# Performance work log

Measured on AMD Instinct MI355X. Metric: run time of the kernel, lower is better.

The kernel has to match this reference:

```python
import jax, jax.numpy as jnp
import numpy as np

N, S, E, D = 20000, 4096, 640000, 256
SPARSITY = 0.02  # fraction of nonzero entries in the normalized matrix


def setup_inputs() -> dict:
    key = jax.random.key(0)
    ks = jax.random.split(key, 6)
    u = jax.random.uniform(ks[0], (N, S), dtype=jnp.float32)
    init = jnp.where(u < SPARSITY, u, 0.0)
    edge_index = jax.random.randint(ks[1], (2, E), 0, N, dtype=jnp.int32)
    edge_attr = jax.random.uniform(ks[2], (E,), dtype=jnp.float32)
    # Projection MLP params (Linear(1,16) -> ReLU -> Linear(16,D))
    w1 = jax.random.normal(ks[3], (1, 16), dtype=jnp.float32)
    b1 = jnp.zeros((16,), dtype=jnp.float32)
    w2 = jax.random.normal(ks[4], (16, D), dtype=jnp.float32) / np.float32(np.sqrt(16))
    b2 = jnp.zeros((D,), dtype=jnp.float32)
    # GCN weight (xavier-ish)
    W = jax.random.normal(ks[5], (D, D), dtype=jnp.float32) / np.float32(np.sqrt(D))
    return {"init": init, "edge_index": edge_index, "edge_attr": edge_attr,
            "w1": w1, "b1": b1, "w2": w2, "b2": b2, "W": W}


def reference(init, edge_index, edge_attr, w1, b1, w2, b2, W):
    n, s = init.shape
    # Projection: torch code feeds the nonzero COLUMN INDICES (as floats) of each
    # row through the MLP and means them. Vectorized: precompute MLP(j) for all
    # column indices j, then do a masked mean via a single matmul.
    idx = jnp.arange(s, dtype=init.dtype)[:, None]          # [S,1]
    phi = jax.nn.relu(idx @ w1 + b1) @ w2 + b2              # [S,D]
    mask = (init != 0).astype(init.dtype)                   # [N,S]
    cnt = mask.sum(axis=1)                                  # [N]
    # rows with zero nonzeros yield zero embedding (matches torch branch)
    h = (mask @ phi) / jnp.maximum(cnt, 1.0)[:, None]       # [N,D]

    # 3-layer GCN: scatter_add of h[row]*attr into col, then mm + relu
    row, col = edge_index[0], edge_index[1]
    for _ in range(3):
        h_agg = jax.ops.segment_sum(h[row] * edge_attr[:, None], col,
                                    num_segments=n)          # [N,D]
        h = jax.nn.relu(h_agg @ W)
    return h
```

## Files before the change

### kernel.cpp

```cpp
#include <hip/hip_runtime.h>


#define N_NODES 20000
#define S_COLS  4096
#define E_EDGES 640000
#define D_DIM   256

typedef unsigned short bf16_t;
typedef __attribute__((ext_vector_type(8))) short short8;
typedef __attribute__((ext_vector_type(4))) float f32x4;

__device__ __forceinline__ float bf2f(bf16_t u) {
    union { unsigned int i; float f; } v; v.i = ((unsigned int)u) << 16; return v.f;
}
__device__ __forceinline__ bf16_t f2bf(float x) {
    union { float f; unsigned int i; } v; v.f = x;
    unsigned int r = v.i + 0x7FFF + ((v.i >> 16) & 1);
    return (bf16_t)(r >> 16);
}
__device__ __forceinline__ float lo_bf(unsigned int u) {
    union { unsigned int i; float f; } v; v.i = u << 16; return v.f;
}
__device__ __forceinline__ float hi_bf(unsigned int u) {
    union { unsigned int i; float f; } v; v.i = u & 0xFFFF0000u; return v.f;
}
__device__ __forceinline__ unsigned int pack_bf(float a, float b) {
    return (unsigned int)f2bf(a) | ((unsigned int)f2bf(b) << 16);
}

__global__ void __launch_bounds__(256, 4)
mega_kernel(const float* __restrict__ init_m,
            const float* __restrict__ w1, const float* __restrict__ b1,
            const float* __restrict__ w2, const float* __restrict__ b2,
            bf16_t* __restrict__ h,
            const int* __restrict__ eidx, int* __restrict__ cnt,
            const float* __restrict__ W,
            bf16_t* __restrict__ Wt_hi, bf16_t* __restrict__ Wt_lo) {
    int b = blockIdx.x;
    int t = threadIdx.x;

    if (b >= 5000) {
        int bb = b - 5000;
        if (bb < 2500) {
            int e = bb * 256 + t;
            atomicAdd(&cnt[eidx[E_EDGES + e]], 1);
        } else {
            int k = bb - 2500;
            float w = W[k * D_DIM + t];
            bf16_t hi = f2bf(w);
            bf16_t lo = f2bf(w - bf2f(hi));
            Wt_hi[t * D_DIM + k] = hi;
            Wt_lo[t * D_DIM + k] = lo;
        }
        return;
    }

    __shared__ float w2s[16][256];
#pragma unroll
    for (int k = 0; k < 16; ++k) w2s[k][t] = w2[k * D_DIM + t];
    __syncthreads();

    int wave = t >> 6, lane = t & 63;
    int row  = b * 4 + wave;

    float lw1[16], lb1[16];
#pragma unroll
    for (int k = 0; k < 16; ++k) { lw1[k] = w1[k]; lb1[k] = b1[k]; }

    const float4* rowp = (const float4*)(init_m + (size_t)row * S_COLS);
    float f[16] = {};
    float cn = 0.f;

#define PROC_COMP(val, jb)                                            \
    if ((val) != 0.f) {                                               \
        float jf = (float)(jb);                                       \
        _Pragma("unroll")                                             \
        for (int k = 0; k < 16; ++k)                                  \
            f[k] += fmaxf(jf * lw1[k] + lb1[k], 0.f);                 \
        cn += 1.f;                                                    \
    }

#pragma unroll 4
    for (int v = 0; v < 16; ++v) {
        float4 x = rowp[v * 64 + lane];
        int jb = (v * 64 + lane) * 4;
        PROC_COMP(x.x, jb)
        PROC_COMP(x.y, jb + 1)
        PROC_COMP(x.z, jb + 2)
        PROC_COMP(x.w, jb + 3)
    }
#undef PROC_COMP

#pragma unroll
    for (int off = 32; off > 0; off >>= 1) {
#pragma unroll
        for (int k = 0; k < 16; ++k) f[k] += __shfl_xor(f[k], off, 64);
        cn += __shfl_xor(cn, off, 64);
    }

    float4 b2v = *(const float4*)(b2 + 4 * lane);
    float o0 = cn * b2v.x, o1 = cn * b2v.y, o2 = cn * b2v.z, o3 = cn * b2v.w;
#pragma unroll
    for (int k = 0; k < 16; ++k) {
        float4 wv = *(const float4*)(&w2s[k][4 * lane]);
        o0 += f[k] * wv.x;  o1 += f[k] * wv.y;
        o2 += f[k] * wv.z;  o3 += f[k] * wv.w;
    }
    float inv = 1.f / fmaxf(cn, 1.f);
    uint2 o;
    o.x = pack_bf(o0 * inv, o1 * inv);
    o.y = pack_bf(o2 * inv, o3 * inv);
    *(uint2*)(h + (size_t)row * D_DIM + 4 * lane) = o;
}

__global__ void scan_kernel(const int* __restrict__ cnt, int* __restrict__ offs,
                            int* __restrict__ cur) {
    __shared__ int sdata[1024];
    int t = threadIdx.x;
    int base = t * 20;
    int vals[20];
    int local = 0;
#pragma unroll
    for (int k = 0; k < 20; ++k) {
        int idx = base + k;
        int v = (idx < N_NODES) ? cnt[idx] : 0;
        vals[k] = local;
        local += v;
    }
    sdata[t] = local;
    __syncthreads();
    for (int off = 1; off < 1024; off <<= 1) {
        int v = (t >= off) ? sdata[t - off] : 0;
        __syncthreads();
        sdata[t] += v;
        __syncthreads();
    }
    int prefix = (t == 0) ? 0 : sdata[t - 1];
#pragma unroll
    for (int k = 0; k < 20; ++k) {
        int idx = base + k;
        if (idx < N_NODES) {
            int o = prefix + vals[k];
            offs[idx] = o;
            cur[idx]  = o;
        }
    }
    if (t == 1023) offs[N_NODES] = sdata[1023];
}

__global__ void fill_kernel(const int* __restrict__ eidx, const float* __restrict__ attr,
                            int* __restrict__ cur, int* __restrict__ src_s,
                            float* __restrict__ attr_s) {
    int e = blockIdx.x * 256 + threadIdx.x;
    if (e < E_EDGES) {
        int r = eidx[e];
        int c = eidx[E_EDGES + e];
        int pos = atomicAdd(&cur[c], 1);
        src_s[pos]  = r;
        attr_s[pos] = attr[e];
    }
}

__global__ void gather_kernel(const bf16_t* __restrict__ h,
                              const int* __restrict__ offs,
                              const int* __restrict__ src_s,
                              const float* __restrict__ attr_s,
                              bf16_t* __restrict__ g) {
    int wid  = (blockIdx.x * blockDim.x + threadIdx.x) >> 6;
    int lane = threadIdx.x & 63;
    if (wid >= N_NODES) return;
    int half = lane >> 5;
    int l32  = lane & 31;
    int e0 = offs[wid], e1 = offs[wid + 1];

    float acc[8] = {};
    for (int base = e0; base < e1; base += 64) {
        int n = e1 - base; if (n > 64) n = 64;
        int   r_l = 0; float a_l = 0.f;
        if (lane < n) { r_l = src_s[base + lane]; a_l = attr_s[base + lane]; }
        int nn = (n + 15) & ~15;
        for (int q = 0; q < nn; q += 16) {
#pragma unroll
            for (int u = 0; u < 8; ++u) {
                int   sl = q + 2 * u + half;
                int   r  = __shfl(r_l, sl, 64);
                float a  = __shfl(a_l, sl, 64);
                uint4 v  = ((const uint4*)(h + (size_t)r * D_DIM))[l32];
                acc[0] += lo_bf(v.x) * a;  acc[1] += hi_bf(v.x) * a;
                acc[2] += lo_bf(v.y) * a;  acc[3] += hi_bf(v.y) * a;
                acc[4] += lo_bf(v.z) * a;  acc[5] += hi_bf(v.z) * a;
                acc[6] += lo_bf(v.w) * a;  acc[7] += hi_bf(v.w) * a;
            }
        }
    }
#pragma unroll
    for (int i = 0; i < 8; ++i) acc[i] += __shfl_xor(acc[i], 32, 64);

    if (half == 0) {
        uint4 o;
        o.x = pack_bf(acc[0], acc[1]);
        o.y = pack_bf(acc[2], acc[3]);
        o.z = pack_bf(acc[4], acc[5]);
        o.w = pack_bf(acc[6], acc[7]);
        ((uint4*)(g + (size_t)wid * D_DIM))[l32] = o;
    }
}

__global__ void __launch_bounds__(256, 2)
gemm_relu_kernel(const bf16_t* __restrict__ g,
                 const bf16_t* __restrict__ Wt_hi,
                 const bf16_t* __restrict__ Wt_lo,
                 bf16_t* __restrict__ hdst, float* __restrict__ fdst) {
    __shared__ bf16_t Bs[64][512];
    int tid  = threadIdx.x;
    int w    = tid >> 6;
    int lane = tid & 63;
    int quad = lane >> 4;
    int id16 = lane & 15;

    int d    = blockIdx.x;
    int xcd  = d & 7;
    int base = (xcd < 4) ? xcd * 79 : 316 + (xcd - 4) * 78;
    int wg   = base + (d >> 3);
    int bx   = wg >> 2;
    int by   = wg & 3;
    int bn   = by * 64;
    int bm0  = bx * 128;

    char* bs = (char*)Bs;

    {
        int tn0 = tid >> 4;
        int ts0 = tid & 15;
#pragma unroll
        for (int it = 0; it < 16; ++it) {
            int n   = tn0 + (it & 3) * 16;
            int seg = ts0 + (it >> 2) * 16;
            const bf16_t* src = (seg < 32 ? Wt_hi : Wt_lo)
                              + (size_t)(bn + n) * D_DIM + (seg & 31) * 8;
            unsigned off = (unsigned)(n * 1024 + seg * 16) ^ (unsigned)((n & 7) << 4);
            *(uint4*)(bs + off) = *(const uint4*)src;
        }
    }

    int r0 = bm0 + w * 32;
    short8 areg[2][8];
#pragma unroll
    for (int j = 0; j < 2; ++j) {
        const bf16_t* arow = g + (size_t)(r0 + j * 16 + id16) * D_DIM;
#pragma unroll
        for (int i = 0; i < 8; ++i)
            areg[j][i] = *(const short8*)(arow + i * 32 + quad * 8);
    }

    __syncthreads();

    unsigned swz   = (unsigned)((id16 & 7) << 4);
    unsigned nbase = (unsigned)(id16 * 1024);

    f32x4 acc[2][4];
#pragma unroll
    for (int j = 0; j < 2; ++j)
#pragma unroll
        for (int nt = 0; nt < 4; ++nt) acc[j][nt] = (f32x4){0.f, 0.f, 0.f, 0.f};

#pragma unroll
    for (int ks = 0; ks < 8; ++ks) {
        unsigned kb = ((unsigned)(ks * 64 + quad * 16)) ^ swz;
#pragma unroll
        for (int nt = 0; nt < 4; ++nt) {
            unsigned off = (unsigned)(nt * 16384) + nbase + kb;
            short8 bh = *(const short8*)(bs + off);
            short8 bl = *(const short8*)(bs + off + 512);
            acc[0][nt] = __builtin_amdgcn_mfma_f32_16x16x32_bf16(areg[0][ks], bh, acc[0][nt], 0, 0, 0);
            acc[0][nt] = __builtin_amdgcn_mfma_f32_16x16x32_bf16(areg[0][ks], bl, acc[0][nt], 0, 0, 0);
            acc[1][nt] = __builtin_amdgcn_mfma_f32_16x16x32_bf16(areg[1][ks], bh, acc[1][nt], 0, 0, 0);
            acc[1][nt] = __builtin_amdgcn_mfma_f32_16x16x32_bf16(areg[1][ks], bl, acc[1][nt], 0, 0, 0);
        }
    }

#pragma unroll
    for (int j = 0; j < 2; ++j) {
#pragma unroll
        for (int nt = 0; nt < 4; ++nt) {
#pragma unroll
            for (int r = 0; r < 4; ++r) {
                int m = r0 + j * 16 + quad * 4 + r;
                if (m < N_NODES) {
                    int n = bn + nt * 16 + id16;
                    float v = fmaxf(acc[j][nt][r], 0.f);
                    if (hdst) hdst[(size_t)m * D_DIM + n] = f2bf(v);
                    else      fdst[(size_t)m * D_DIM + n] = v;
                }
            }
        }
    }
}

extern "C" void kernel_launch(void* const* d_in, const int* in_sizes, int n_in,
                              void* d_out, int out_size, void* d_ws, size_t ws_size,
                              hipStream_t stream) {
    const float* init_m = (const float*)d_in[0];
    const int*   eidx   = (const int*)  d_in[1];
    const float* attr   = (const float*)d_in[2];
    const float* w1     = (const float*)d_in[3];
    const float* b1     = (const float*)d_in[4];
    const float* w2     = (const float*)d_in[5];
    const float* b2     = (const float*)d_in[6];
    const float* Wm     = (const float*)d_in[7];
    float* out = (float*)d_out;

    char* ws = (char*)d_ws;
    bf16_t* hbuf   = (bf16_t*)ws;
    bf16_t* gbuf   = (bf16_t*)(ws + 10240000);
    int*    cnt    = (int*)   (ws + 20529152);
    int*    offs   = (int*)   (ws + 20609152);
    int*    cur    = (int*)   (ws + 20689408);
    int*    src_s  = (int*)   (ws + 20769408);
    float*  attr_s = (float*) (ws + 23329408);
    bf16_t* Wt_hi  = (bf16_t*)(ws + 25889408);
    bf16_t* Wt_lo  = (bf16_t*)(ws + 26020480);

    hipMemsetAsync(ws + 20480000, 0, 129152, stream);

    mega_kernel<<<5000 + 2500 + 256, 256, 0, stream>>>(
        init_m, w1, b1, w2, b2, hbuf, eidx, cnt, Wm, Wt_hi, Wt_lo);
    scan_kernel<<<1, 1024, 0, stream>>>(cnt, offs, cur);
    fill_kernel<<<(E_EDGES + 255) / 256, 256, 0, stream>>>(eidx, attr, cur, src_s, attr_s);

    dim3 ggrid((N_NODES * 64 + 255) / 256);
    for (int it = 0; it < 3; ++it) {
        gather_kernel<<<ggrid, 256, 0, stream>>>(hbuf, offs, src_s, attr_s, gbuf);
        if (it == 2)
            gemm_relu_kernel<<<628, 256, 0, stream>>>(gbuf, Wt_hi, Wt_lo,
                                                      (bf16_t*)nullptr, out);
        else
            gemm_relu_kernel<<<628, 256, 0, stream>>>(gbuf, Wt_hi, Wt_lo,
                                                      hbuf, (float*)nullptr);
    }
}
```

Before: 694.3 us.

## Compute masked projection mean with bf16 MFMA against precomputed split-bf16 phi table

Precomputes relu(j*w1+b1) for every column index in a small kernel, stored as hi/lo bf16 pairs. The projection stage then builds 0/1 mask fragments from init and accumulates mask@phi plus the row count with MFMA instructions, 16 rows per block. The wave partial sums are reduced in shared memory before the w2/b2 stage. This replaces per-nonzero scalar FMA loops with divergent branches by matrix-core work, while the 328MB read of init stays the same. It adds one kernel launch, and the split-bf16 table may lose a little precision.

New measurement: 684.7 us. Within noise of the previous version (-1.4%).

```diff
diff --git a/kernel.cpp b/kernel.cpp
--- a/kernel.cpp
+++ b/kernel.cpp
@@ -28,10 +28,24 @@
     return (unsigned int)f2bf(a) | ((unsigned int)f2bf(b) << 16);
 }
 
+__global__ void pphi_kernel(const float* __restrict__ w1, const float* __restrict__ b1,
+                            bf16_t* __restrict__ Pt_hi, bf16_t* __restrict__ Pt_lo) {
+    int j = blockIdx.x * 256 + threadIdx.x;
+    float jf = (float)j;
+#pragma unroll
+    for (int f = 0; f < 16; ++f) {
+        float phi = fmaxf(jf * w1[f] + b1[f], 0.f);
+        bf16_t hi = f2bf(phi);
+        bf16_t lo = f2bf(phi - bf2f(hi));
+        Pt_hi[f * S_COLS + j] = hi;
+        Pt_lo[f * S_COLS + j] = lo;
+    }
+}
+
 __global__ void __launch_bounds__(256, 4)
 mega_kernel(const float* __restrict__ init_m,
-            const float* __restrict__ w1, const float* __restrict__ b1,
             const float* __restrict__ w2, const float* __restrict__ b2,
+            const bf16_t* __restrict__ Pt_hi, const bf16_t* __restrict__ Pt_lo,
             bf16_t* __restrict__ h,
             const int* __restrict__ eidx, int* __restrict__ cnt,
             const float* __restrict__ W,
@@ -39,8 +53,8 @@
     int b = blockIdx.x;
     int t = threadIdx.x;
 
-    if (b >= 5000) {
-        int bb = b - 5000;
+    if (b >= 1250) {
+        int bb = b - 1250;
         if (bb < 2500) {
             int e = bb * 256 + t;
             atomicAdd(&cnt[eidx[E_EDGES + e]], 1);
@@ -56,61 +70,94 @@
     }
 
     __shared__ float w2s[16][256];
+    __shared__ float Fred[4][16][16];
+    __shared__ float Cred[4][16];
+
 #pragma unroll
     for (int k = 0; k < 16; ++k) w2s[k][t] = w2[k * D_DIM + t];
+
+    int wave = t >> 6, lane = t & 63;
+    int quad = lane >> 4, id16 = lane & 15;
+    int r0 = b * 16;
+
+    const float*  arow = init_m + (size_t)(r0 + id16) * S_COLS + wave * 1024 + quad * 8;
+    const bf16_t* bph  = Pt_hi + id16 * S_COLS + wave * 1024 + quad * 8;
+    const bf16_t* bpl  = Pt_lo + id16 * S_COLS + wave * 1024 + quad * 8;
+
+    short8 bones;
+    short ov = (id16 == 0) ? (short)0x3F80 : (short)0;
+#pragma unroll
+    for (int i = 0; i < 8; ++i) bones[i] = ov;
+
+    f32x4 accF = (f32x4){0.f, 0.f, 0.f, 0.f};
+    f32x4 accC = (f32x4){0.f, 0.f, 0.f, 0.f};
+
+    const short M1 = (short)0x3F80;
+#pragma unroll 4
+    for (int s = 0; s < 32; ++s) {
+        float4 x0 = *(const float4*)(arow + s * 32);
+        float4 x1 = *(const float4*)(arow + s * 32 + 4);
+        short8 bh = *(const short8*)(bph + s * 32);
+        short8 bl = *(const short8*)(bpl + s * 32);
+        short8 a;
+        a[0] = (x0.x != 0.f) ? M1 : (short)0;
+        a[1] = (x0.y != 0.f) ? M1 : (short)0;
+        a[2] = (x0.z != 0.f) ? M1 : (short)0;
+        a[3] = (x0.w != 0.f) ? M1 : (short)0;
+        a[4] = (x1.x != 0.f) ? M1 : (short)0;
+        a[5] = (x1.y != 0.f) ? M1 : (short)0;
+        a[6] = (x1.z != 0.f) ? M1 : (short)0;
+        a[7] = (x1.w != 0.f) ? M1 : (short)0;
+        accF = __builtin_amdgcn_mfma_f32_16x16x32_bf16(a, bh, accF, 0, 0, 0);
+        accF = __builtin_amdgcn_mfma_f32_16x16x32_bf16(a, bl, accF, 0, 0, 0);
+        accC = __builtin_amdgcn_mfma_f32_16x16x32_bf16(a, bones, accC, 0, 0, 0);
+    }
+
+#pragma unroll
+    for (int r = 0; r < 4; ++r)
+        Fred[wave][quad * 4 + r][id16] = accF[r];
+    if (id16 == 0) {
+#pragma unroll
+        for (int r = 0; r < 4; ++r)
+            Cred[wave][quad * 4 + r] = accC[r];
+    }
     __syncthreads();
 
-    int wave = t >> 6, lane = t & 63;
-    int row  = b * 4 + wave;
-
-    float lw1[16], lb1[16];
-#pragma unroll
-    for (int k = 0; k < 16; ++k) { lw1[k] = w1[k]; lb1[k] = b1[k]; }
-
-    const float4* rowp = (const float4*)(init_m + (size_t)row * S_COLS);
-    float f[16] = {};
-    float cn = 0.f;
-
-#define PROC_COMP(val, jb)                                            \
-    if ((val) != 0.f) {                                               \
-        float jf = (float)(jb);                                       \
-        _Pragma("unroll")                                             \
-        for (int k = 0; k < 16; ++k)                                  \
-            f[k] += fmaxf(jf * lw1[k] + lb1[k], 0.f);                 \
-        cn += 1.f;                                                    \
-    }
-
-#pragma unroll 4
-    for (int v = 0; v < 16; ++v) {
-        float4 x = rowp[v * 64 + lane];
-        int jb = (v * 64 + lane) * 4;
-        PROC_COMP(x.x, jb)
-        PROC_COMP(x.y, jb + 1)
-        PROC_COMP(x.z, jb + 2)
-        PROC_COMP(x.w, jb + 3)
-    }
-#undef PROC_COMP
-
-#pragma unroll
-    for (int off = 32; off > 0; off >>= 1) {
-#pragma unroll
-        for (int k = 0; k < 16; ++k) f[k] += __shfl_xor(f[k], off, 64);
-        cn += __shfl_xor(cn, off, 64);
-    }
-
-    float4 b2v = *(const float4*)(b2 + 4 * lane);
-    float o0 = cn * b2v.x, o1 = cn * b2v.y, o2 = cn * b2v.z, o3 = cn * b2v.w;
-#pragma unroll
-    for (int k = 0; k < 16; ++k) {
-        float4 wv = *(const float4*)(&w2s[k][4 * lane]);
-        o0 += f[k] * wv.x;  o1 += f[k] * wv.y;
-        o2 += f[k] * wv.z;  o3 += f[k] * wv.w;
-    }
+    int row = t >> 4, cg = t & 15;
+    float Frow[16];
+#pragma unroll
+    for (int f = 0; f < 16; ++f)
+        Frow[f] = Fred[0][row][f] + Fred[1][row][f] + Fred[2][row][f] + Fred[3][row][f];
+    float cn = Cred[0][row] + Cred[1][row] + Cred[2][row] + Cred[3][row];
     float inv = 1.f / fmaxf(cn, 1.f);
-    uint2 o;
-    o.x = pack_bf(o0 * inv, o1 * inv);
-    o.y = pack_bf(o2 * inv, o3 * inv);
-    *(uint2*)(h + (size_t)row * D_DIM + 4 * lane) = o;
+
+    int c0 = cg * 16;
+    float o[16];
+#pragma unroll
+    for (int jj = 0; jj < 4; ++jj) {
+        float4 bv = *(const float4*)(b2 + c0 + jj * 4);
+        o[jj * 4 + 0] = cn * bv.x;  o[jj * 4 + 1] = cn * bv.y;
+        o[jj * 4 + 2] = cn * bv.z;  o[jj * 4 + 3] = cn * bv.w;
+    }
+#pragma unroll
+    for (int f = 0; f < 16; ++f) {
+        float fv = Frow[f];
+#pragma unroll
+        for (int jj = 0; jj < 16; ++jj)
+            o[jj] += fv * w2s[f][c0 + jj];
+    }
+    uint4 p0, p1;
+    p0.x = pack_bf(o[0] * inv,  o[1] * inv);
+    p0.y = pack_bf(o[2] * inv,  o[3] * inv);
+    p0.z = pack_bf(o[4] * inv,  o[5] * inv);
+    p0.w = pack_bf(o[6] * inv,  o[7] * inv);
+    p1.x = pack_bf(o[8] * inv,  o[9] * inv);
+    p1.y = pack_bf(o[10] * inv, o[11] * inv);
+    p1.z = pack_bf(o[12] * inv, o[13] * inv);
+    p1.w = pack_bf(o[14] * inv, o[15] * inv);
+    uint4* dst = (uint4*)(h + (size_t)(r0 + row) * D_DIM + c0);
+    dst[0] = p0;
+    dst[1] = p1;
 }
 
 __global__ void scan_kernel(const int* __restrict__ cnt, int* __restrict__ offs,
@@ -320,11 +367,15 @@
     float*  attr_s = (float*) (ws + 23329408);
     bf16_t* Wt_hi  = (bf16_t*)(ws + 25889408);
     bf16_t* Wt_lo  = (bf16_t*)(ws + 26020480);
+    bf16_t* Pt_hi  = (bf16_t*)(ws + 26151552);
+    bf16_t* Pt_lo  = (bf16_t*)(ws + 26282624);
 
     hipMemsetAsync(ws + 20480000, 0, 129152, stream);
 
-    mega_kernel<<<5000 + 2500 + 256, 256, 0, stream>>>(
-        init_m, w1, b1, w2, b2, hbuf, eidx, cnt, Wm, Wt_hi, Wt_lo);
+    pphi_kernel<<<16, 256, 0, stream>>>(w1, b1, Pt_hi, Pt_lo);
+
+    mega_kernel<<<1250 + 2500 + 256, 256, 0, stream>>>(
+        init_m, w2, b2, Pt_hi, Pt_lo, hbuf, eidx, cnt, Wm, Wt_hi, Wt_lo);
     scan_kernel<<<1, 1024, 0, stream>>>(cnt, offs, cur);
     fill_kernel<<<(E_EDGES + 255) / 256, 256, 0, stream>>>(eidx, attr, cur, src_s, attr_s);
 
```
